# Performance work log

Hardware: AMD Instinct MI355X
Metric: run time of the kernel (lower is better)

Reference implementation:

```python
import jax, jax.numpy as jnp
import numpy as np

N, P, E, H = 64, 1024, 512, 8
R = E // H  # head dim


def _xavier(key, shape, dtype=jnp.float32):
    fan_in, fan_out = shape[-1], shape[-2] if len(shape) > 1 else shape[-1]
    lim = jnp.sqrt(6.0 / (fan_in + fan_out)).astype(dtype)
    return jax.random.uniform(key, shape, dtype, -lim, lim)


def setup_inputs() -> dict:
    key = jax.random.key(0)
    k1, k2, k3, k4 = jax.random.split(key, 4)
    x = jax.random.normal(k1, (N, P, E), dtype=jnp.float32)
    alpha = _xavier(k2, (H, P))          # translation-invariant attention weights
    V = _xavier(k3, (H, R, E))           # per-head value projection
    W = _xavier(k4, (E, E))              # Dense kernel
    b = jnp.zeros((E,), dtype=jnp.float32)  # Dense bias
    return {"x": x, "alpha": alpha, "V": V, "W": W, "b": b}


def _log_cosh(x):
    # log(cosh(x)) = |x| + log1p(exp(-2|x|)) - log(2), numerically stable
    ax = jnp.abs(x)
    return ax + jnp.log1p(jnp.exp(-2.0 * ax)) - jnp.log(2.0).astype(x.dtype)


def reference(x, alpha, V, W, b):
    n, p, e = x.shape
    # circulant matrix: alpha_mat[h, i, j] = alpha[h, (j - i) mod P]
    # (equivalent to stacking jnp.roll(alpha, shift=i) over i)
    idx = (jnp.arange(p)[None, :] - jnp.arange(p)[:, None]) % p  # (P, P)
    alpha_mat = alpha[:, idx]                                    # (H, P, P)
    ws = jnp.einsum('hrd,npd->nhpr', V, x)                       # (N, H, P, R)
    y = jnp.einsum('hpj,nhjr->nphr', alpha_mat, ws)              # (N, P, H, R)
    y = y.reshape(n, p, -1)                                      # (N, P, E)
    y = y @ W + b
    return _log_cosh(y)
```

## Files before the change

kernel.cpp:

```cpp
#include <hip/hip_runtime.h>
#include <math.h>

typedef float f32x4 __attribute__((ext_vector_type(4)));
typedef __bf16 bf16x8 __attribute__((ext_vector_type(8)));
typedef unsigned short u16x8 __attribute__((ext_vector_type(8)));
typedef unsigned short u16x4 __attribute__((ext_vector_type(4)));

#define LN2F_ 0.69314718055994530942f

__device__ inline unsigned short f2bf(float f) {
    unsigned u = __builtin_bit_cast(unsigned, f);
    u += 0x7fffu + ((u >> 16) & 1u);
    return (unsigned short)(u >> 16);
}

__device__ inline void stage_st(unsigned short* Ls, int row, int c, u16x8 v) {
    *(u16x8*)(Ls + (row >> 4) * 512 + (((c) << 4) + ((row & 15) ^ ((c) << 1))) * 8) = v;
}
__device__ inline bf16x8 frag_ld(const unsigned short* Ls, int s, int ml, int q) {
    return __builtin_bit_cast(bf16x8,
        *(const u16x8*)(Ls + s * 512 + (((q) << 4) + (ml ^ ((q) << 1))) * 8));
}

__global__ __launch_bounds__(256) void k_cvt(const float* __restrict__ in,
                                             unsigned short* __restrict__ out, int n4) {
    int i = blockIdx.x * 256 + threadIdx.x;
    if (i >= n4) return;
    float4 v = ((const float4*)in)[i];
    u16x4 o = { f2bf(v.x), f2bf(v.y), f2bf(v.z), f2bf(v.w) };
    *(u16x4*)(out + (size_t)i * 4) = o;
}

__global__ __launch_bounds__(256) void k_build_am(const float* __restrict__ alpha,
                                                  unsigned short* __restrict__ am) {
    int t = blockIdx.x * 256 + threadIdx.x;
    int j8 = (t & 127) << 3;
    int p  = (t >> 7) & 1023;
    int h  = t >> 17;
    const float* ar = alpha + (h << 10);
    u16x8 o;
#pragma unroll
    for (int q = 0; q < 8; ++q) o[q] = f2bf(ar[(j8 + q - p) & 1023]);
    *(u16x8*)(am + ((size_t)t << 3)) = o;
}

__global__ __launch_bounds__(256) void k_build_wt(const float* __restrict__ W,
                                                  unsigned short* __restrict__ WT) {
    int t = blockIdx.x * 256 + threadIdx.x;
    int e1 = t >> 9, e = t & 511;
    WT[t] = f2bf(W[e * 512 + e1]);
}

__global__ __launch_bounds__(256) void k_gemm1(const float* __restrict__ X,
                                               const unsigned short* __restrict__ B,
                                               unsigned short* __restrict__ wsT) {
    __shared__ __align__(16) unsigned short As[128 * 32];
    __shared__ __align__(16) unsigned short Bs[128 * 32];
    const int tid = threadIdx.x;
    const int m0 = blockIdx.y * 128;
    const int e0 = blockIdx.x * 128;
    const int w = tid >> 6, lane = tid & 63, ml = lane & 15, quad = lane >> 4;
    const int wr = w >> 1, wc = w & 1;
    const int srow = tid >> 1, shalf = tid & 1;
    f32x4 acc[4][4] = {};
    for (int k0 = 0; k0 < 512; k0 += 32) {
        const float* ap = X + (size_t)(m0 + srow) * 512 + k0 + shalf * 16;
        float4 a0 = ((const float4*)ap)[0];
        float4 a1 = ((const float4*)ap)[1];
        float4 a2 = ((const float4*)ap)[2];
        float4 a3 = ((const float4*)ap)[3];
        const unsigned short* bp = B + (size_t)(e0 + srow) * 512 + k0 + shalf * 16;
        u16x8 rb0 = *(const u16x8*)bp;
        u16x8 rb1 = *(const u16x8*)(bp + 8);
        __syncthreads();
        u16x8 pa0 = { f2bf(a0.x), f2bf(a0.y), f2bf(a0.z), f2bf(a0.w),
                      f2bf(a1.x), f2bf(a1.y), f2bf(a1.z), f2bf(a1.w) };
        u16x8 pa1 = { f2bf(a2.x), f2bf(a2.y), f2bf(a2.z), f2bf(a2.w),
                      f2bf(a3.x), f2bf(a3.y), f2bf(a3.z), f2bf(a3.w) };
        stage_st(As, srow, shalf * 2 + 0, pa0);
        stage_st(As, srow, shalf * 2 + 1, pa1);
        stage_st(Bs, srow, shalf * 2 + 0, rb0);
        stage_st(Bs, srow, shalf * 2 + 1, rb1);
        __syncthreads();
        bf16x8 af[4], bfr[4];
#pragma unroll
        for (int i = 0; i < 4; ++i) {
            af[i]  = frag_ld(As, wr * 4 + i, ml, quad);
            bfr[i] = frag_ld(Bs, wc * 4 + i, ml, quad);
        }
#pragma unroll
        for (int i = 0; i < 4; ++i)
#pragma unroll
            for (int j = 0; j < 4; ++j)
                acc[i][j] = __builtin_amdgcn_mfma_f32_16x16x32_bf16(af[i], bfr[j], acc[i][j], 0, 0, 0);
    }
    const int n = m0 >> 10;
    const int pblk = m0 & 1023;
#pragma unroll
    for (int i = 0; i < 4; ++i) {
        int p = pblk + wr * 64 + i * 16 + quad * 4;
#pragma unroll
        for (int j = 0; j < 4; ++j) {
            int e = e0 + wc * 64 + j * 16 + ml;
            u16x4 o = { f2bf(acc[i][j][0]), f2bf(acc[i][j][1]),
                        f2bf(acc[i][j][2]), f2bf(acc[i][j][3]) };
            *(u16x4*)(wsT + ((size_t)n * 512 + e) * 1024 + p) = o;
        }
    }
}

__global__ __launch_bounds__(256) void k_gemm2(const unsigned short* __restrict__ wsT,
                                               const unsigned short* __restrict__ am,
                                               unsigned short* __restrict__ y) {
    __shared__ __align__(16) unsigned short As[64 * 32];
    __shared__ __align__(16) unsigned short Bs[128 * 32];
    const int tid = threadIdx.x;
    const int p0 = blockIdx.x * 128;
    const int h  = blockIdx.y;
    const int n  = blockIdx.z;
    const int w = tid >> 6, lane = tid & 63, ml = lane & 15, quad = lane >> 4;
    const int wr = w >> 1, wc = w & 1;
    const int arow = tid >> 2, ac = tid & 3;
    const int brow = tid >> 1, bhalf = tid & 1;
    const unsigned short* Abase = wsT + (size_t)n * 524288 + (size_t)(h * 64) * 1024;
    const unsigned short* Bbase = am + ((size_t)h * 1024 + p0) * 1024;
    f32x4 acc[2][4] = {};
    for (int j0 = 0; j0 < 1024; j0 += 32) {
        u16x8 ra  = *(const u16x8*)(Abase + (size_t)arow * 1024 + j0 + ac * 8);
        const unsigned short* bp = Bbase + (size_t)brow * 1024 + j0 + bhalf * 16;
        u16x8 rb0 = *(const u16x8*)bp;
        u16x8 rb1 = *(const u16x8*)(bp + 8);
        __syncthreads();
        stage_st(As, arow, ac, ra);
        stage_st(Bs, brow, bhalf * 2 + 0, rb0);
        stage_st(Bs, brow, bhalf * 2 + 1, rb1);
        __syncthreads();
        bf16x8 af[2], bfr[4];
#pragma unroll
        for (int mt = 0; mt < 2; ++mt)
            af[mt] = frag_ld(As, wr * 2 + mt, ml, quad);
#pragma unroll
        for (int nt = 0; nt < 4; ++nt)
            bfr[nt] = frag_ld(Bs, wc * 4 + nt, ml, quad);
#pragma unroll
        for (int mt = 0; mt < 2; ++mt)
#pragma unroll
            for (int nt = 0; nt < 4; ++nt)
                acc[mt][nt] = __builtin_amdgcn_mfma_f32_16x16x32_bf16(af[mt], bfr[nt], acc[mt][nt], 0, 0, 0);
    }
#pragma unroll
    for (int mt = 0; mt < 2; ++mt) {
        int r0 = wr * 32 + mt * 16 + quad * 4;
#pragma unroll
        for (int nt = 0; nt < 4; ++nt) {
            int p = p0 + wc * 64 + nt * 16 + ml;
            u16x4 o = { f2bf(acc[mt][nt][0]), f2bf(acc[mt][nt][1]),
                        f2bf(acc[mt][nt][2]), f2bf(acc[mt][nt][3]) };
            *(u16x4*)(y + ((size_t)n * 1024 + p) * 512 + h * 64 + r0) = o;
        }
    }
}

__global__ __launch_bounds__(256) void k_gemm3(const unsigned short* __restrict__ A,
                                               const unsigned short* __restrict__ B,
                                               const float* __restrict__ bias,
                                               float* __restrict__ out) {
    __shared__ __align__(16) unsigned short As[128 * 32];
    __shared__ __align__(16) unsigned short Bs[128 * 32];
    const int tid = threadIdx.x;
    const int m0 = blockIdx.y * 128;
    const int e0 = blockIdx.x * 128;
    const int w = tid >> 6, lane = tid & 63, ml = lane & 15, quad = lane >> 4;
    const int wr = w >> 1, wc = w & 1;
    const int srow = tid >> 1, shalf = tid & 1;
    f32x4 acc[4][4] = {};
    for (int k0 = 0; k0 < 512; k0 += 32) {
        const unsigned short* ap = A + (size_t)(m0 + srow) * 512 + k0 + shalf * 16;
        u16x8 ra0 = *(const u16x8*)ap;
        u16x8 ra1 = *(const u16x8*)(ap + 8);
        const unsigned short* bp = B + (size_t)(e0 + srow) * 512 + k0 + shalf * 16;
        u16x8 rb0 = *(const u16x8*)bp;
        u16x8 rb1 = *(const u16x8*)(bp + 8);
        __syncthreads();
        stage_st(As, srow, shalf * 2 + 0, ra0);
        stage_st(As, srow, shalf * 2 + 1, ra1);
        stage_st(Bs, srow, shalf * 2 + 0, rb0);
        stage_st(Bs, srow, shalf * 2 + 1, rb1);
        __syncthreads();
        bf16x8 af[4], bfr[4];
#pragma unroll
        for (int i = 0; i < 4; ++i) {
            af[i]  = frag_ld(As, wr * 4 + i, ml, quad);
            bfr[i] = frag_ld(Bs, wc * 4 + i, ml, quad);
        }
#pragma unroll
        for (int i = 0; i < 4; ++i)
#pragma unroll
            for (int j = 0; j < 4; ++j)
                acc[i][j] = __builtin_amdgcn_mfma_f32_16x16x32_bf16(af[i], bfr[j], acc[i][j], 0, 0, 0);
    }
#pragma unroll
    for (int j = 0; j < 4; ++j) {
        int e = e0 + wc * 64 + j * 16 + ml;
        float bv = bias[e];
#pragma unroll
        for (int i = 0; i < 4; ++i) {
            int mg = m0 + wr * 64 + i * 16 + quad * 4;
#pragma unroll
            for (int r = 0; r < 4; ++r) {
                float v  = acc[i][j][r] + bv;
                float ax = fabsf(v);
                float t  = __expf(-2.0f * ax);
                out[(size_t)(mg + r) * 512 + e] = ax + __logf(1.0f + t) - LN2F_;
            }
        }
    }
}

extern "C" void kernel_launch(void* const* d_in, const int* in_sizes, int n_in,
                              void* d_out, int out_size, void* d_ws, size_t ws_size,
                              hipStream_t stream) {
    const float* x     = (const float*)d_in[0];
    const float* alpha = (const float*)d_in[1];
    const float* V     = (const float*)d_in[2];
    const float* W     = (const float*)d_in[3];
    const float* b     = (const float*)d_in[4];

    unsigned short* am  = (unsigned short*)d_out;
    unsigned short* Vb  = am + 8388608;
    unsigned short* wsT = (unsigned short*)d_ws;
    unsigned short* y   = wsT + 33554432;
    unsigned short* WT  = wsT;
    float* out = (float*)d_out;

    k_cvt<<<256, 256, 0, stream>>>(V, Vb, 65536);
    k_build_am<<<4096, 256, 0, stream>>>(alpha, am);

    k_gemm1<<<dim3(4, 512), 256, 0, stream>>>(x, Vb, wsT);
    k_gemm2<<<dim3(8, 8, 64), 256, 0, stream>>>(wsT, am, y);
    k_build_wt<<<1024, 256, 0, stream>>>(W, WT);
    k_gemm3<<<dim3(4, 512), 256, 0, stream>>>(y, WT, b, out);
}
```

Baseline: 527.9 us.

## Batch four samples per block in circulant GEMM to reuse alpha tiles

The circulant-matrix GEMM now handles four batch samples per 512-thread block, so each loaded tile of the bf16 circulant alpha matrix is shared across four samples' ws tiles instead of being reloaded per sample. Each wave computes a 64x64 output tile (4x4 MFMA fragments) for one sample, which doubles the accumulator registers per thread. The grid shrinks to a quarter of the blocks. The intent is to cut global and L2 traffic on the circulant matrix, at the cost of lower occupancy and fewer blocks.

```diff
diff --git a/kernel.cpp b/kernel.cpp
--- a/kernel.cpp
+++ b/kernel.cpp
@@ -109,51 +109,52 @@
     }
 }
 
-__global__ __launch_bounds__(256) void k_gemm2(const unsigned short* __restrict__ wsT,
+__global__ __launch_bounds__(512) void k_gemm2(const unsigned short* __restrict__ wsT,
                                                const unsigned short* __restrict__ am,
                                                unsigned short* __restrict__ y) {
-    __shared__ __align__(16) unsigned short As[64 * 32];
+    __shared__ __align__(16) unsigned short As[256 * 32];
     __shared__ __align__(16) unsigned short Bs[128 * 32];
     const int tid = threadIdx.x;
     const int p0 = blockIdx.x * 128;
     const int h  = blockIdx.y;
-    const int n  = blockIdx.z;
+    const int n0 = blockIdx.z * 4;
     const int w = tid >> 6, lane = tid & 63, ml = lane & 15, quad = lane >> 4;
-    const int wr = w >> 1, wc = w & 1;
-    const int arow = tid >> 2, ac = tid & 3;
-    const int brow = tid >> 1, bhalf = tid & 1;
-    const unsigned short* Abase = wsT + (size_t)n * 524288 + (size_t)(h * 64) * 1024;
-    const unsigned short* Bbase = am + ((size_t)h * 1024 + p0) * 1024;
-    f32x4 acc[2][4] = {};
+    const int wn = w >> 1, wp = w & 1;
+    const int arow = tid >> 1, ahalf = tid & 1;
+    const int brow = tid >> 2, bc = tid & 3;
+    const unsigned short* Ap = wsT + (size_t)(n0 + (arow >> 6)) * 524288
+                                   + (size_t)(h * 64 + (arow & 63)) * 1024 + ahalf * 16;
+    const unsigned short* Bp = am + ((size_t)h * 1024 + p0 + brow) * 1024 + bc * 8;
+    f32x4 acc[4][4] = {};
     for (int j0 = 0; j0 < 1024; j0 += 32) {
-        u16x8 ra  = *(const u16x8*)(Abase + (size_t)arow * 1024 + j0 + ac * 8);
-        const unsigned short* bp = Bbase + (size_t)brow * 1024 + j0 + bhalf * 16;
-        u16x8 rb0 = *(const u16x8*)bp;
-        u16x8 rb1 = *(const u16x8*)(bp + 8);
-        __syncthreads();
-        stage_st(As, arow, ac, ra);
-        stage_st(Bs, brow, bhalf * 2 + 0, rb0);
-        stage_st(Bs, brow, bhalf * 2 + 1, rb1);
-        __syncthreads();
-        bf16x8 af[2], bfr[4];
-#pragma unroll
-        for (int mt = 0; mt < 2; ++mt)
-            af[mt] = frag_ld(As, wr * 2 + mt, ml, quad);
+        u16x8 ra0 = *(const u16x8*)(Ap + j0);
+        u16x8 ra1 = *(const u16x8*)(Ap + j0 + 8);
+        u16x8 rb  = *(const u16x8*)(Bp + j0);
+        __syncthreads();
+        stage_st(As, arow, ahalf * 2 + 0, ra0);
+        stage_st(As, arow, ahalf * 2 + 1, ra1);
+        stage_st(Bs, brow, bc, rb);
+        __syncthreads();
+        bf16x8 af[4], bfr[4];
+#pragma unroll
+        for (int mt = 0; mt < 4; ++mt)
+            af[mt] = frag_ld(As, wn * 4 + mt, ml, quad);
 #pragma unroll
         for (int nt = 0; nt < 4; ++nt)
-            bfr[nt] = frag_ld(Bs, wc * 4 + nt, ml, quad);
-#pragma unroll
-        for (int mt = 0; mt < 2; ++mt)
+            bfr[nt] = frag_ld(Bs, wp * 4 + nt, ml, quad);
+#pragma unroll
+        for (int mt = 0; mt < 4; ++mt)
 #pragma unroll
             for (int nt = 0; nt < 4; ++nt)
                 acc[mt][nt] = __builtin_amdgcn_mfma_f32_16x16x32_bf16(af[mt], bfr[nt], acc[mt][nt], 0, 0, 0);
     }
-#pragma unroll
-    for (int mt = 0; mt < 2; ++mt) {
-        int r0 = wr * 32 + mt * 16 + quad * 4;
+    const int n = n0 + wn;
+#pragma unroll
+    for (int mt = 0; mt < 4; ++mt) {
+        int r0 = mt * 16 + quad * 4;
 #pragma unroll
         for (int nt = 0; nt < 4; ++nt) {
-            int p = p0 + wc * 64 + nt * 16 + ml;
+            int p = p0 + wp * 64 + nt * 16 + ml;
             u16x4 o = { f2bf(acc[mt][nt][0]), f2bf(acc[mt][nt][1]),
                         f2bf(acc[mt][nt][2]), f2bf(acc[mt][nt][3]) };
             *(u16x4*)(y + ((size_t)n * 1024 + p) * 512 + h * 64 + r0) = o;
@@ -237,7 +238,7 @@
     k_build_am<<<4096, 256, 0, stream>>>(alpha, am);
 
     k_gemm1<<<dim3(4, 512), 256, 0, stream>>>(x, Vb, wsT);
-    k_gemm2<<<dim3(8, 8, 64), 256, 0, stream>>>(wsT, am, y);
+    k_gemm2<<<dim3(8, 8, 16), 512, 0, stream>>>(wsT, am, y);
     k_build_wt<<<1024, 256, 0, stream>>>(W, WT);
     k_gemm3<<<dim3(4, 512), 256, 0, stream>>>(y, WT, b, out);
 }
```

New measurement: 482.9 us. 1.09x faster.
